# Optimization experiments

Hardware: AMD Instinct MI355X
Metric: run time of the kernel (lower is better)

Reference implementation:

```python
import jax, jax.numpy as jnp
import numpy as np

B, L, S, M, N = 128, 3, 256, 256, 20000
NS, A, NL = 4, 5, 2
MAP_RANGE = 10.0
DELTA_VAR = 0.1
EPS = 1e-5


def _ln(x):
    mu = jnp.mean(x, -1, keepdims=True)
    var = jnp.var(x, -1, keepdims=True)
    return (x - mu) / jnp.sqrt(var + EPS)


def _cal_map_last(map_pts, anchor_last):
    # map_pts: [2, N], anchor_last: [B, 1, L] -> [B, M, 2]
    pos = anchor_last[:, 0, 0:2]
    d = map_pts[None, :, :] - pos[:, :, None]                    # [B,2,N]
    th = anchor_last[:, 0, -1]
    c, s = jnp.cos(th), jnp.sin(th)
    rot = jnp.stack([jnp.stack([c, s], -1), jnp.stack([-s, c], -1)], 1)  # [B,2,2]
    m = jnp.einsum('bij,bjn->bin', rot, d)                       # ego-frame points
    dis = jnp.sqrt(jnp.sum(m * m, axis=1, keepdims=True))        # [B,1,N]
    m = jnp.where(dis >= MAP_RANGE, 1e10, m)
    m = jnp.sort(m, axis=-1)                                     # per-coordinate sort (as in torch)
    m = jnp.where(m >= 1e9, 0.0, m)
    m = m[:, :, :M]                                              # torch F.pad negative pad == crop to map_num_max
    return jnp.transpose(m, (0, 2, 1))


def _forward(inp_start_point, map_pts, end_point, delta_limit_mean,
             W_enc_anchor, Wq, Wk, Wv, W_in, W_out, W_map1, W_map2,
             W_ih0, W_ih1, W_hh0, W_hh1, W_m1, W_m2, W_v1, W_v2):
    anchor = inp_start_point
    var_last = jnp.ones_like(anchor) * 0.01  # never updated, as in torch source
    pre_mean, pre_var, views = [], [], []
    scale = 1.0 / np.sqrt(S)                 # MHA 1 head -> head_dim = S
    bsz = anchor.shape[0]
    for step in range(NS):
        dm, dv = [anchor], [var_last]
        vt = [jnp.transpose(_cal_map_last(map_pts, anchor), (0, 2, 1))]
        h = jnp.ones((NL, bsz, S), anchor.dtype)
        c = jnp.ones((NL, bsz, S), anchor.dtype)
        for _ in range(A - 1):
            enc_a = _ln(jnp.concatenate([anchor, anchor - end_point, var_last], -1) @ W_enc_anchor[step].T)  # [B,1,S]
            ml = jax.lax.stop_gradient(_cal_map_last(map_pts, anchor))  # torch.no_grad in encode_last_map
            q = ml @ Wq[step].T
            k = ml @ Wk[step].T
            v = ml @ Wv[step].T
            wq, wk, wv = jnp.split(W_in[step], 3, axis=0)
            q2 = q @ wq.T
            k2 = k @ wk.T
            v2 = v @ wv.T
            attn = jax.nn.softmax(jnp.einsum('bqs,bks->bqk', q2, k2) * scale, axis=-1)
            o = jnp.einsum('bqk,bks->bqs', attn, v2) @ W_out[step].T    # [B,M,S]
            x = jax.nn.relu(jnp.transpose(o, (0, 2, 1)))                # [B,S,M]
            x = jax.nn.relu(x @ W_map1[step].T) @ W_map2[step].T        # [B,S,1]
            enc_m = _ln(jnp.transpose(x, (0, 2, 1)))                    # [B,1,S]
            xl = jnp.concatenate([enc_a, enc_m], -1)[:, 0, :]           # [B,2S], single LSTM timestep
            hs, cs = [], []
            for l, (Wih, Whh) in enumerate(((W_ih0[step], W_hh0[step]), (W_ih1[step], W_hh1[step]))):
                g = xl @ Wih.T + h[l] @ Whh.T
                i_g, f_g, g_g, o_g = jnp.split(g, 4, -1)               # torch gate order i,f,g,o
                cl = jax.nn.sigmoid(f_g) * c[l] + jax.nn.sigmoid(i_g) * jnp.tanh(g_g)
                hl = jax.nn.sigmoid(o_g) * jnp.tanh(cl)
                hs.append(hl)
                cs.append(cl)
                xl = hl
            h, c = jnp.stack(hs), jnp.stack(cs)
            mn = _ln(xl)[:, None, :]                                    # [B,1,S]
            mean = jnp.tanh(jax.nn.relu(jax.nn.relu(mn) @ W_m1[step].T) @ W_m2[step].T) * delta_limit_mean + anchor
            varr = jax.nn.sigmoid(jax.nn.relu(jax.nn.relu(mn) @ W_v1[step].T) @ W_v2[step].T) * DELTA_VAR
            dm.append(mean)
            dv.append(varr)
            anchor = mean
            vt.append(jnp.transpose(_cal_map_last(map_pts, anchor), (0, 2, 1)))
        pre_mean.append(jnp.concatenate(dm, 1)[:, None])    # [B,1,A,L]
        pre_var.append(jnp.concatenate(dv, 1)[:, None])
        views.append(jnp.stack(vt, 1)[:, None])             # [B,1,A,2,M]
    return (jnp.concatenate(pre_mean, 1), jnp.concatenate(pre_var, 1), jnp.concatenate(views, 1))


def setup_inputs() -> dict:
    key = jax.random.key(0)
    ks = jax.random.split(key, 20)

    def w(k, shape, fan):
        return jax.random.normal(k, shape, jnp.float32) / np.sqrt(fan)

    return {
        'inp_start_point': jax.random.normal(ks[0], (B, 1, L), jnp.float32) * 2.0,
        'map_pts': jax.random.uniform(ks[1], (2, N), jnp.float32, -50.0, 50.0),
        'end_point': jnp.array([5.0, 5.0, 0.0], jnp.float32),
        'delta_limit_mean': jnp.array([1.0, 1.0, 0.3], jnp.float32),
        'W_enc_anchor': w(ks[2], (NS, S, 3 * L), 3 * L),
        'Wq': w(ks[3], (NS, S, 2), 2),
        'Wk': w(ks[4], (NS, S, 2), 2),
        'Wv': w(ks[5], (NS, S, 2), 2),
        'W_in': w(ks[6], (NS, 3 * S, S), S),
        'W_out': w(ks[7], (NS, S, S), S),
        'W_map1': w(ks[8], (NS, S, M), M),
        'W_map2': w(ks[9], (NS, 1, S), S),
        'W_ih0': w(ks[10], (NS, 4 * S, 2 * S), 2 * S),
        'W_ih1': w(ks[11], (NS, 4 * S, S), S),
        'W_hh0': w(ks[12], (NS, 4 * S, S), S),
        'W_hh1': w(ks[13], (NS, 4 * S, S), S),
        'W_m1': w(ks[14], (NS, S, S), S),
        'W_m2': w(ks[15], (NS, L, S), S),
        'W_v1': w(ks[16], (NS, S, S), S),
        'W_v2': w(ks[17], (NS, L, S), S),
    }


def reference(inp_start_point, map_pts, end_point, delta_limit_mean,
              W_enc_anchor, Wq, Wk, Wv, W_in, W_out, W_map1, W_map2,
              W_ih0, W_ih1, W_hh0, W_hh1, W_m1, W_m2, W_v1, W_v2):
    return _forward(inp_start_point, map_pts, end_point, delta_limit_mean,
                    W_enc_anchor, Wq, Wk, Wv, W_in, W_out, W_map1, W_map2,
                    W_ih0, W_ih1, W_hh0, W_hh1, W_m1, W_m2, W_v1, W_v2)
```

## Files before the change

kernel.cpp:

```cpp
#include <hip/hip_runtime.h>

#define BB 128
#define NPTS 20000
#define NSTEP 4
#define NITER 4

#define OFF_ANCHOR 0
#define OFF_G      384
#define OFF_AO     400
#define OFF_U      2448
#define OFF_XL     67984
#define OFF_OUT    133520
#define OFF_H      166288
#define OFF_C      231824
#define OFF_GB     297360
#define OFF_RMN    428432
#define OFF_TM     461200
#define OFF_TV     493968

#define OUT_VAR   7680
#define OUT_VIEWS 15360

__device__ __forceinline__ float sigf(float x){ return 1.0f/(1.0f+expf(-x)); }

__device__ __forceinline__ float blockSum256(float v, float* buf){
    for (int off = 32; off > 0; off >>= 1) v += __shfl_down(v, off, 64);
    int tid = threadIdx.x;
    __syncthreads();
    if ((tid & 63) == 0) buf[tid >> 6] = v;
    __syncthreads();
    return (buf[0] + buf[1]) + (buf[2] + buf[3]);
}

__device__ __forceinline__ double blockSum256d(double v, double* buf){
    for (int off = 32; off > 0; off >>= 1) v += __shfl_down(v, off, 64);
    int tid = threadIdx.x;
    __syncthreads();
    if ((tid & 63) == 0) buf[tid >> 6] = v;
    __syncthreads();
    return (buf[0] + buf[1]) + (buf[2] + buf[3]);
}

__global__ __launch_bounds__(256) void k_init(const float* __restrict__ inp, float* __restrict__ ws)
{
    int i = blockIdx.x*256 + threadIdx.x;
    if (i < BB*3) ws[OFF_ANCHOR + i] = inp[i];
}

__global__ __launch_bounds__(256) void k_pre(const float* __restrict__ Wq, const float* __restrict__ Wk,
                                             const float* __restrict__ Wv, const float* __restrict__ Win,
                                             const float* __restrict__ Wout, float* __restrict__ ws)
{
    __shared__ float wql[512], wkl[512], wvl[512];
    __shared__ double avl[512];
    __shared__ double dbuf[4];
    int s = blockIdx.x, t = threadIdx.x;
    wql[t] = Wq[s*512 + t];   wql[256+t] = Wq[s*512 + 256 + t];
    wkl[t] = Wk[s*512 + t];   wkl[256+t] = Wk[s*512 + 256 + t];
    wvl[t] = Wv[s*512 + t];   wvl[256+t] = Wv[s*512 + 256 + t];
    __syncthreads();
    const float* wq = Win + s*196608 + t*256;
    const float* wk = wq + 65536;
    const float* wv = wq + 131072;
    double aq0=0,aq1=0,ak0=0,ak1=0,av0=0,av1=0;
    for (int j = 0; j < 256; j++){
        double a = wq[j], b = wk[j], c = wv[j];
        aq0 += a*(double)wql[j*2]; aq1 += a*(double)wql[j*2+1];
        ak0 += b*(double)wkl[j*2]; ak1 += b*(double)wkl[j*2+1];
        av0 += c*(double)wvl[j*2]; av1 += c*(double)wvl[j*2+1];
    }
    avl[t*2] = av0; avl[t*2+1] = av1;
    double g00 = blockSum256d(aq0*ak0, dbuf);
    double g01 = blockSum256d(aq0*ak1, dbuf);
    double g10 = blockSum256d(aq1*ak0, dbuf);
    double g11 = blockSum256d(aq1*ak1, dbuf);
    if (t == 0){
        ws[OFF_G + s*4+0] = (float)g00; ws[OFF_G + s*4+1] = (float)g01;
        ws[OFF_G + s*4+2] = (float)g10; ws[OFF_G + s*4+3] = (float)g11;
    }
    const float* wo = Wout + s*65536 + t*256;
    double o0 = 0.0, o1 = 0.0;
    for (int j = 0; j < 256; j++){
        double w = wo[j];
        o0 += w*avl[j*2]; o1 += w*avl[j*2+1];
    }
    ws[OFF_AO + s*512 + t*2]   = (float)o0;
    ws[OFF_AO + s*512 + t*2+1] = (float)o1;
}

__global__ __launch_bounds__(256) void k_step_init(float* __restrict__ ws, float* __restrict__ out, int s)
{
    int gid = blockIdx.x*256 + threadIdx.x;
    if (gid < 2*BB*256){ ws[OFF_H + gid] = 1.0f; ws[OFF_C + gid] = 1.0f; }
    if (gid < BB*3){
        int b = gid/3, j = gid - b*3;
        out[((b*NSTEP + s)*5 + 0)*3 + j] = ws[OFF_ANCHOR + gid];
        out[OUT_VAR + ((b*NSTEP + s)*5 + 0)*3 + j] = 0.01f;
    }
}

__global__ __launch_bounds__(256) void k_map(const float* __restrict__ mp, float* __restrict__ ws,
                                             float* __restrict__ out, int s, int t)
{
    __shared__ unsigned int histx[2048], histy[2048];
    __shared__ float vx[1024], vy[1024];
    __shared__ float candx[512], candy[512];
    __shared__ float sortx[256], sorty[256];
    __shared__ int scanb[256];
    __shared__ int shjx, shjy;
    __shared__ unsigned int cnt_in, cntx, cnty;
    int tid = threadIdx.x, b = blockIdx.x;
    float ax = ws[OFF_ANCHOR + b*3 + 0];
    float ay = ws[OFF_ANCHOR + b*3 + 1];
    float th = ws[OFF_ANCHOR + b*3 + 2];
    float cth = cosf(th), sth = sinf(th);
    for (int i = tid; i < 2048; i += 256){ histx[i] = 0u; histy[i] = 0u; }
    if (tid == 0){ cnt_in = 0u; cntx = 0u; cnty = 0u; }
    __syncthreads();
    for (int i = tid; i < NPTS; i += 256){
        float dx = mp[i] - ax, dy = mp[NPTS + i] - ay;
        float rx = cth*dx + sth*dy;
        float ry = cth*dy - sth*dx;
        float d  = sqrtf(rx*rx + ry*ry);
        if (d < 10.0f){
            unsigned p = atomicAdd(&cnt_in, 1u);
            if (p < 1024u){ vx[p] = rx; vy[p] = ry; }
            int bx = (int)((rx + 10.0f) * 102.4f); bx = min(max(bx, 0), 2047);
            int by = (int)((ry + 10.0f) * 102.4f); by = min(max(by, 0), 2047);
            atomicAdd(&histx[bx], 1u); atomicAdd(&histy[by], 1u);
        }
    }
    __syncthreads();
    int total = (int)min(cnt_in, 1024u);
    int K = min(256, total);
    {
        int part = 0;
        for (int k = 0; k < 8; k++) part += (int)histx[tid*8 + k];
        scanb[tid] = part; __syncthreads();
        for (int off = 1; off < 256; off <<= 1){
            int v = (tid >= off) ? scanb[tid - off] : 0; __syncthreads();
            scanb[tid] += v; __syncthreads();
        }
        int incl = scanb[tid], excl = incl - part;
        if (K > 0 && excl < K && incl >= K){
            int c = excl;
            for (int k = 0; k < 8; k++){ c += (int)histx[tid*8+k]; if (c >= K){ shjx = tid*8+k; break; } }
        }
        if (K == 0 && tid == 0) shjx = -1;
        __syncthreads();
    }
    {
        int part = 0;
        for (int k = 0; k < 8; k++) part += (int)histy[tid*8 + k];
        scanb[tid] = part; __syncthreads();
        for (int off = 1; off < 256; off <<= 1){
            int v = (tid >= off) ? scanb[tid - off] : 0; __syncthreads();
            scanb[tid] += v; __syncthreads();
        }
        int incl = scanb[tid], excl = incl - part;
        if (K > 0 && excl < K && incl >= K){
            int c = excl;
            for (int k = 0; k < 8; k++){ c += (int)histy[tid*8+k]; if (c >= K){ shjy = tid*8+k; break; } }
        }
        if (K == 0 && tid == 0) shjy = -1;
        __syncthreads();
    }
    int jx = shjx, jy = shjy;
    for (int i = tid; i < total; i += 256){
        float v = vx[i];
        int bx = (int)((v + 10.0f)*102.4f); bx = min(max(bx,0),2047);
        if (bx <= jx){ unsigned p = atomicAdd(&cntx,1u); if (p < 512u) candx[p] = v; }
        v = vy[i];
        int by = (int)((v + 10.0f)*102.4f); by = min(max(by,0),2047);
        if (by <= jy){ unsigned p = atomicAdd(&cnty,1u); if (p < 512u) candy[p] = v; }
    }
    __syncthreads();
    int cx = (int)min(cntx, 512u), cy = (int)min(cnty, 512u);
    for (int i = tid; i < cx; i += 256){
        float v = candx[i];
        int r = 0;
        for (int j = 0; j < cx; j++){
            float w = candx[j];
            r += (w < v) || (w == v && j < i);
        }
        if (r < 256) sortx[r] = v;
    }
    for (int i = tid; i < cy; i += 256){
        float v = candy[i];
        int r = 0;
        for (int j = 0; j < cy; j++){
            float w = candy[j];
            r += (w < v) || (w == v && j < i);
        }
        if (r < 256) sorty[r] = v;
    }
    __syncthreads();
    int obase = OUT_VIEWS + (((b*NSTEP + s)*5 + t)*2)*256;
    out[obase + tid]       = (tid < K) ? sortx[tid] : 0.0f;
    out[obase + 256 + tid] = (tid < K) ? sorty[tid] : 0.0f;
}

__global__ __launch_bounds__(256) void k_encattn(const float* __restrict__ out, float* __restrict__ ws,
                                                 const float* __restrict__ Wenc, const float* __restrict__ endp,
                                                 int s, int t)
{
    __shared__ float rbuf[4];
    __shared__ float mlx[256], mly[256];
    int b = blockIdx.x, i = threadIdx.x;
    int obase = OUT_VIEWS + (((b*NSTEP + s)*5 + t)*2)*256;
    mlx[i] = out[obase + i];
    mly[i] = out[obase + 256 + i];
    float a0 = ws[OFF_ANCHOR + b*3+0], a1 = ws[OFF_ANCHOR + b*3+1], a2 = ws[OFF_ANCHOR + b*3+2];
    float z[9] = {a0, a1, a2, a0-endp[0], a1-endp[1], a2-endp[2], 0.01f, 0.01f, 0.01f};
    const float* w = Wenc + s*2304 + i*9;
    float acc = 0.f;
    #pragma unroll
    for (int j = 0; j < 9; j++) acc += z[j]*w[j];
    float mu = blockSum256(acc, rbuf) * (1.0f/256.0f);
    float d = acc - mu;
    float var = blockSum256(d*d, rbuf) * (1.0f/256.0f);
    ws[OFF_XL + b*512 + i] = d * rsqrtf(var + 1e-5f);
    float g00 = ws[OFF_G + s*4+0], g01 = ws[OFF_G + s*4+1];
    float g10 = ws[OFF_G + s*4+2], g11 = ws[OFF_G + s*4+3];
    float x = mlx[i], y = mly[i];
    float t0 = g00*x + g10*y;
    float t1 = g01*x + g11*y;
    float mx = -1e30f;
    for (int j = 0; j < 256; j++){
        float l = (t0*mlx[j] + t1*mly[j]) * 0.0625f;
        mx = fmaxf(mx, l);
    }
    float sum = 0.f, ux = 0.f, uy = 0.f;
    for (int j = 0; j < 256; j++){
        float l = (t0*mlx[j] + t1*mly[j]) * 0.0625f;
        float e = expf(l - mx);
        sum += e; ux += e*mlx[j]; uy += e*mly[j];
    }
    float inv = 1.0f/sum;
    ws[OFF_U + b*512 + i*2]   = ux*inv;
    ws[OFF_U + b*512 + i*2+1] = uy*inv;
}

__global__ __launch_bounds__(256) void k_big(float* __restrict__ ws, const float* __restrict__ W1,
                                             const float* __restrict__ W2, int s)
{
    __shared__ __align__(16) float ul[512];
    __shared__ float aol[128];
    __shared__ float w2l[64];
    __shared__ __align__(16) float xt[64*36];
    __shared__ __align__(16) float w1t[64*36];
    __shared__ float red[64*17];
    int sct = blockIdx.x, st = blockIdx.y, b = blockIdx.z;
    int tid = threadIdx.x, tx = tid & 15, ty = tid >> 4;
    {
        float2 uv = *(const float2*)(ws + OFF_U + b*512 + tid*2);
        ul[tid*2] = uv.x; ul[tid*2+1] = uv.y;
        if (tid < 128) aol[tid] = ws[OFF_AO + s*512 + st*128 + tid];
        if (tid < 64)  w2l[tid] = W2[sct*64 + tid];
    }
    __syncthreads();
    float acc[4][4];
    #pragma unroll
    for (int i=0;i<4;i++){
        #pragma unroll
        for (int j=0;j<4;j++) acc[i][j] = 0.f;
    }
    for (int mt = 0; mt < 8; mt++){
        {
            int cl = tid >> 2, f0 = tid & 3;
            const float* g = W1 + (sct*64 + cl)*256 + mt*32 + f0*4;
            float4 v0 = *(const float4*)g;
            float4 v1 = *(const float4*)(g + 16);
            *(float4*)(w1t + cl*36 + f0*4)      = v0;
            *(float4*)(w1t + cl*36 + f0*4 + 16) = v1;
        }
        {
            int r = tid >> 2, mg = tid & 3;
            float A0 = aol[r*2], A1 = aol[r*2+1];
            int m0 = mt*32 + mg*4;
            float4 o0, o1;
            o0.x = fmaxf(A0*ul[(m0+0)*2] + A1*ul[(m0+0)*2+1], 0.f);
            o0.y = fmaxf(A0*ul[(m0+1)*2] + A1*ul[(m0+1)*2+1], 0.f);
            o0.z = fmaxf(A0*ul[(m0+2)*2] + A1*ul[(m0+2)*2+1], 0.f);
            o0.w = fmaxf(A0*ul[(m0+3)*2] + A1*ul[(m0+3)*2+1], 0.f);
            int m1 = mt*32 + (mg+4)*4;
            o1.x = fmaxf(A0*ul[(m1+0)*2] + A1*ul[(m1+0)*2+1], 0.f);
            o1.y = fmaxf(A0*ul[(m1+1)*2] + A1*ul[(m1+1)*2+1], 0.f);
            o1.z = fmaxf(A0*ul[(m1+2)*2] + A1*ul[(m1+2)*2+1], 0.f);
            o1.w = fmaxf(A0*ul[(m1+3)*2] + A1*ul[(m1+3)*2+1], 0.f);
            *(float4*)(xt + r*36 + mg*4)     = o0;
            *(float4*)(xt + r*36 + (mg+4)*4) = o1;
        }
        __syncthreads();
        #pragma unroll
        for (int m4 = 0; m4 < 8; m4++){
            float4 xv[4], wv[4];
            #pragma unroll
            for (int i=0;i<4;i++) xv[i] = *(const float4*)(xt + (ty*4+i)*36 + m4*4);
            #pragma unroll
            for (int j=0;j<4;j++) wv[j] = *(const float4*)(w1t + (tx + 16*j)*36 + m4*4);
            #pragma unroll
            for (int i=0;i<4;i++){
                #pragma unroll
                for (int j=0;j<4;j++){
                    acc[i][j] += xv[i].x*wv[j].x + xv[i].y*wv[j].y + xv[i].z*wv[j].z + xv[i].w*wv[j].w;
                }
            }
        }
        __syncthreads();
    }
    float psum[4];
    #pragma unroll
    for (int i=0;i<4;i++){
        float p = 0.f;
        #pragma unroll
        for (int j=0;j<4;j++) p += fmaxf(acc[i][j], 0.f) * w2l[tx + 16*j];
        psum[i] = p;
        red[(ty*4+i)*17 + tx] = p;
    }
    __syncthreads();
    if (tid < 64){
        float sm = 0.f;
        #pragma unroll
        for (int q=0;q<16;q++) sm += red[tid*17 + q];
        ws[OFF_GB + b*1024 + sct*256 + st*64 + tid] = sm;
    }
}

__global__ __launch_bounds__(256) void k_lnencm(float* __restrict__ ws)
{
    __shared__ float rbuf[4];
    int b = blockIdx.x, t = threadIdx.x;
    const float* p = ws + OFF_GB + b*1024;
    float v = ((p[t] + p[256+t]) + p[512+t]) + p[768+t];
    v = p[t];
    v += p[256+t]; v += p[512+t]; v += p[768+t];
    float mu = blockSum256(v, rbuf) * (1.0f/256.0f);
    float d = v - mu;
    float var = blockSum256(d*d, rbuf) * (1.0f/256.0f);
    ws[OFF_XL + b*512 + 256 + t] = d * rsqrtf(var + 1e-5f);
}

template<int K>
__device__ __forceinline__ void gemm_pass(const float* __restrict__ A, const float* __restrict__ W,
                                          float* As, float* Wsh, float (&acc)[2][4],
                                          int bt, int ot, int tid)
{
    int tx = tid & 15, ty = tid >> 4;
    for (int kt = 0; kt < K/32; kt++){
        {
            int bb = tid >> 3, kk = (tid & 7) * 4;
            float4 v = *(const float4*)(A + (bt*32+bb)*K + kt*32 + kk);
            float* ap = As + bb*33 + kk;
            ap[0]=v.x; ap[1]=v.y; ap[2]=v.z; ap[3]=v.w;
        }
        {
            int oo = tid >> 2, kk = (tid & 3) * 8;
            const float* g = W + (ot*64+oo)*K + kt*32 + kk;
            float4 v0 = *(const float4*)g;
            float4 v1 = *(const float4*)(g + 4);
            float* wp = Wsh + oo*33 + kk;
            wp[0]=v0.x; wp[1]=v0.y; wp[2]=v0.z; wp[3]=v0.w;
            wp[4]=v1.x; wp[5]=v1.y; wp[6]=v1.z; wp[7]=v1.w;
        }
        __syncthreads();
        #pragma unroll
        for (int kk = 0; kk < 32; kk++){
            float a0 = As[(ty*2)*33 + kk], a1 = As[(ty*2+1)*33 + kk];
            float w0 = Wsh[(tx*4)*33+kk],   w1 = Wsh[(tx*4+1)*33+kk];
            float w2 = Wsh[(tx*4+2)*33+kk], w3 = Wsh[(tx*4+3)*33+kk];
            acc[0][0] += a0*w0; acc[0][1] += a0*w1; acc[0][2] += a0*w2; acc[0][3] += a0*w3;
            acc[1][0] += a1*w0; acc[1][1] += a1*w1; acc[1][2] += a1*w2; acc[1][3] += a1*w3;
        }
        __syncthreads();
    }
}

template<int K1, int K2, int RELU>
__global__ __launch_bounds__(256) void k_gemm(const float* __restrict__ A1, const float* __restrict__ W1,
                                              const float* __restrict__ A2, const float* __restrict__ W2,
                                              float* __restrict__ C, int Osz)
{
    __shared__ float As[32*33];
    __shared__ float Wsh[64*33];
    int tid = threadIdx.x, tx = tid & 15, ty = tid >> 4;
    int ot = blockIdx.x, bt = blockIdx.y;
    float acc[2][4];
    #pragma unroll
    for (int i=0;i<2;i++){
        #pragma unroll
        for (int j=0;j<4;j++) acc[i][j]=0.f;
    }
    gemm_pass<K1>(A1, W1, As, Wsh, acc, bt, ot, tid);
    if constexpr (K2 > 0){
        gemm_pass<K2>(A2, W2, As, Wsh, acc, bt, ot, tid);
    }
    #pragma unroll
    for (int i=0;i<2;i++){
        float4 v;
        v.x = acc[i][0]; v.y = acc[i][1]; v.z = acc[i][2]; v.w = acc[i][3];
        if (RELU){ v.x=fmaxf(v.x,0.f); v.y=fmaxf(v.y,0.f); v.z=fmaxf(v.z,0.f); v.w=fmaxf(v.w,0.f); }
        *(float4*)(C + (bt*32+ty*2+i)*Osz + ot*64 + tx*4) = v;
    }
}

__global__ __launch_bounds__(256) void k_heads2(const float* __restrict__ A, const float* __restrict__ Wm1,
                                                const float* __restrict__ Wv1, float* __restrict__ ws)
{
    __shared__ float As[32*33];
    __shared__ float Wsh[64*33];
    int tid = threadIdx.x, tx = tid & 15, ty = tid >> 4;
    int bx = blockIdx.x, bt = blockIdx.y;
    int ot = bx & 3;
    const float* W = (bx < 4) ? Wm1 : Wv1;
    float* C = ws + ((bx < 4) ? OFF_TM : OFF_TV);
    float acc[2][4];
    #pragma unroll
    for (int i=0;i<2;i++){
        #pragma unroll
        for (int j=0;j<4;j++) acc[i][j]=0.f;
    }
    gemm_pass<256>(A, W, As, Wsh, acc, bt, ot, tid);
    #pragma unroll
    for (int i=0;i<2;i++){
        float4 v;
        v.x = fmaxf(acc[i][0],0.f); v.y = fmaxf(acc[i][1],0.f);
        v.z = fmaxf(acc[i][2],0.f); v.w = fmaxf(acc[i][3],0.f);
        *(float4*)(C + (bt*32+ty*2+i)*256 + ot*64 + tx*4) = v;
    }
}

__global__ __launch_bounds__(256) void k_gates(float* __restrict__ ws, int l)
{
    int b = blockIdx.x, t = threadIdx.x;
    const float* g = ws + OFF_GB + b*1024;
    float ig = g[t], fg = g[256+t], gg = g[512+t], og = g[768+t];
    int idx = l*BB*256 + b*256 + t;
    float cold = ws[OFF_C + idx];
    float cl = sigf(fg)*cold + sigf(ig)*tanhf(gg);
    float hl = sigf(og)*tanhf(cl);
    ws[OFF_C + idx] = cl;
    ws[OFF_H + idx] = hl;
}

__global__ __launch_bounds__(256) void k_mn(float* __restrict__ ws)
{
    __shared__ float rbuf[4];
    int b = blockIdx.x, t = threadIdx.x;
    const float* g = ws + OFF_GB + b*1024;
    float ig = g[t], fg = g[256+t], gg = g[512+t], og = g[768+t];
    int idx = BB*256 + b*256 + t;
    float cold = ws[OFF_C + idx];
    float cl = sigf(fg)*cold + sigf(ig)*tanhf(gg);
    float hl = sigf(og)*tanhf(cl);
    ws[OFF_C + idx] = cl;
    ws[OFF_H + idx] = hl;
    float mu = blockSum256(hl, rbuf) * (1.0f/256.0f);
    float d = hl - mu;
    float var = blockSum256(d*d, rbuf) * (1.0f/256.0f);
    ws[OFF_RMN + b*256 + t] = fmaxf(d * rsqrtf(var + 1e-5f), 0.0f);
}

__global__ __launch_bounds__(256) void k_head(const float* __restrict__ Wm2, const float* __restrict__ Wv2,
                                              const float* __restrict__ dlm, float* __restrict__ ws,
                                              float* __restrict__ out, int s, int t)
{
    int b = blockIdx.x, tid = threadIdx.x;
    int w = tid >> 6, lane = tid & 63;
    #pragma unroll
    for (int p = 0; p < 2; p++){
        int oi = p*4 + w;
        if (oi < 6){
            int j = (oi < 3) ? oi : oi - 3;
            const float* tb = ws + ((oi < 3) ? OFF_TM : OFF_TV) + b*256;
            const float* wr = ((oi < 3) ? Wm2 : Wv2) + j*256;
            float pa = 0.f;
            #pragma unroll
            for (int q = 0; q < 4; q++) pa += tb[lane + 64*q] * wr[lane + 64*q];
            for (int off = 32; off > 0; off >>= 1) pa += __shfl_down(pa, off, 64);
            if (lane == 0){
                if (oi < 3){
                    float mv = tanhf(pa) * dlm[j] + ws[OFF_ANCHOR + b*3 + j];
                    out[((b*NSTEP + s)*5 + (t+1))*3 + j] = mv;
                    ws[OFF_ANCHOR + b*3 + j] = mv;
                } else {
                    out[OUT_VAR + ((b*NSTEP + s)*5 + (t+1))*3 + j] = sigf(pa)*0.1f;
                }
            }
        }
    }
}

extern "C" void kernel_launch(void* const* d_in, const int* in_sizes, int n_in,
                              void* d_out, int out_size, void* d_ws, size_t ws_size,
                              hipStream_t stream)
{
    (void)in_sizes; (void)n_in; (void)out_size; (void)ws_size;
    const float* inp  = (const float*)d_in[0];
    const float* mp   = (const float*)d_in[1];
    const float* endp = (const float*)d_in[2];
    const float* dlm  = (const float*)d_in[3];
    const float* Wenc = (const float*)d_in[4];
    const float* Wq   = (const float*)d_in[5];
    const float* Wk   = (const float*)d_in[6];
    const float* Wv   = (const float*)d_in[7];
    const float* Win  = (const float*)d_in[8];
    const float* Wout = (const float*)d_in[9];
    const float* Wmap1= (const float*)d_in[10];
    const float* Wmap2= (const float*)d_in[11];
    const float* Wih0 = (const float*)d_in[12];
    const float* Wih1 = (const float*)d_in[13];
    const float* Whh0 = (const float*)d_in[14];
    const float* Whh1 = (const float*)d_in[15];
    const float* Wm1  = (const float*)d_in[16];
    const float* Wm2  = (const float*)d_in[17];
    const float* Wv1  = (const float*)d_in[18];
    const float* Wv2  = (const float*)d_in[19];
    float* out = (float*)d_out;
    float* ws  = (float*)d_ws;

    k_init<<<2, 256, 0, stream>>>(inp, ws);
    k_pre<<<NSTEP, 256, 0, stream>>>(Wq, Wk, Wv, Win, Wout, ws);
    for (int s = 0; s < NSTEP; s++){
        k_step_init<<<256, 256, 0, stream>>>(ws, out, s);
        for (int t = 0; t < NITER; t++){
            k_map<<<BB, 256, 0, stream>>>(mp, ws, out, s, t);
            k_encattn<<<BB, 256, 0, stream>>>(out, ws, Wenc, endp, s, t);
            k_big<<<dim3(4, 4, BB), 256, 0, stream>>>(ws, Wmap1 + s*65536, Wmap2 + s*256, s);
            k_lnencm<<<BB, 256, 0, stream>>>(ws);
            k_gemm<512,256,0><<<dim3(16,4), 256, 0, stream>>>(ws+OFF_XL, Wih0 + s*524288,
                                                              ws+OFF_H,  Whh0 + s*262144,
                                                              ws+OFF_GB, 1024);
            k_gates<<<BB, 256, 0, stream>>>(ws, 0);
            k_gemm<256,256,0><<<dim3(16,4), 256, 0, stream>>>(ws+OFF_H,          Wih1 + s*262144,
                                                              ws+OFF_H + BB*256, Whh1 + s*262144,
                                                              ws+OFF_GB, 1024);
            k_mn<<<BB, 256, 0, stream>>>(ws);
            k_heads2<<<dim3(8,4), 256, 0, stream>>>(ws+OFF_RMN, Wm1 + s*65536, Wv1 + s*65536, ws);
            k_head<<<BB, 256, 0, stream>>>(Wm2 + s*768, Wv2 + s*768, dlm, ws, out, s, t);
        }
        k_map<<<BB, 256, 0, stream>>>(mp, ws, out, s, 4);
    }
}
```

Baseline: 4.492 ms.

## Fuse map sort with encoder/attention, coarsen histogram, enlarge k_big tiles

The map selection kernel, the encoder/attention kernel and the per-step init are merged into one kernel, so the views no longer round-trip through global memory. The final map of each step is now computed by the next step's first launch, which writes it to both slots. The radix histogram drops from 2048 to 256 bins with a single scan, and the candidate buffer shrinks to 448. k_big moves to 128x128 tiles with an 8x8 register tile per thread, which cuts the grid from 16 to 4 blocks per batch row but raises register pressure, and a coarser histogram risks candidate overflow.

```diff
diff --git a/kernel.cpp b/kernel.cpp
--- a/kernel.cpp
+++ b/kernel.cpp
@@ -10,7 +10,6 @@
 #define OFF_AO     400
 #define OFF_U      2448
 #define OFF_XL     67984
-#define OFF_OUT    133520
 #define OFF_H      166288
 #define OFF_C      231824
 #define OFF_GB     297360
@@ -88,33 +87,24 @@
     ws[OFF_AO + s*512 + t*2+1] = (float)o1;
 }
 
-__global__ __launch_bounds__(256) void k_step_init(float* __restrict__ ws, float* __restrict__ out, int s)
-{
-    int gid = blockIdx.x*256 + threadIdx.x;
-    if (gid < 2*BB*256){ ws[OFF_H + gid] = 1.0f; ws[OFF_C + gid] = 1.0f; }
-    if (gid < BB*3){
-        int b = gid/3, j = gid - b*3;
-        out[((b*NSTEP + s)*5 + 0)*3 + j] = ws[OFF_ANCHOR + gid];
-        out[OUT_VAR + ((b*NSTEP + s)*5 + 0)*3 + j] = 0.01f;
-    }
-}
-
-__global__ __launch_bounds__(256) void k_map(const float* __restrict__ mp, float* __restrict__ ws,
-                                             float* __restrict__ out, int s, int t)
-{
-    __shared__ unsigned int histx[2048], histy[2048];
+__global__ __launch_bounds__(256) void k_mapenc(const float* __restrict__ mp, float* __restrict__ ws,
+                                                float* __restrict__ out, const float* __restrict__ Wenc,
+                                                const float* __restrict__ endp, int s, int t, int wprev)
+{
+    __shared__ unsigned int histx[256], histy[256];
     __shared__ float vx[1024], vy[1024];
-    __shared__ float candx[512], candy[512];
-    __shared__ float sortx[256], sorty[256];
-    __shared__ int scanb[256];
+    __shared__ float candx[448], candy[448];
+    __shared__ float mxS[256], myS[256];
+    __shared__ int scanx[256], scany[256];
     __shared__ int shjx, shjy;
     __shared__ unsigned int cnt_in, cntx, cnty;
+    __shared__ float rbuf[4];
     int tid = threadIdx.x, b = blockIdx.x;
     float ax = ws[OFF_ANCHOR + b*3 + 0];
     float ay = ws[OFF_ANCHOR + b*3 + 1];
     float th = ws[OFF_ANCHOR + b*3 + 2];
     float cth = cosf(th), sth = sinf(th);
-    for (int i = tid; i < 2048; i += 256){ histx[i] = 0u; histy[i] = 0u; }
+    histx[tid] = 0u; histy[tid] = 0u;
     if (tid == 0){ cnt_in = 0u; cntx = 0u; cnty = 0u; }
     __syncthreads();
     for (int i = tid; i < NPTS; i += 256){
@@ -125,205 +115,201 @@
         if (d < 10.0f){
             unsigned p = atomicAdd(&cnt_in, 1u);
             if (p < 1024u){ vx[p] = rx; vy[p] = ry; }
-            int bx = (int)((rx + 10.0f) * 102.4f); bx = min(max(bx, 0), 2047);
-            int by = (int)((ry + 10.0f) * 102.4f); by = min(max(by, 0), 2047);
+            int bx = min(max((int)((rx + 10.0f)*12.8f), 0), 255);
+            int by = min(max((int)((ry + 10.0f)*12.8f), 0), 255);
             atomicAdd(&histx[bx], 1u); atomicAdd(&histy[by], 1u);
         }
     }
     __syncthreads();
     int total = (int)min(cnt_in, 1024u);
     int K = min(256, total);
-    {
-        int part = 0;
-        for (int k = 0; k < 8; k++) part += (int)histx[tid*8 + k];
-        scanb[tid] = part; __syncthreads();
-        for (int off = 1; off < 256; off <<= 1){
-            int v = (tid >= off) ? scanb[tid - off] : 0; __syncthreads();
-            scanb[tid] += v; __syncthreads();
-        }
-        int incl = scanb[tid], excl = incl - part;
-        if (K > 0 && excl < K && incl >= K){
-            int c = excl;
-            for (int k = 0; k < 8; k++){ c += (int)histx[tid*8+k]; if (c >= K){ shjx = tid*8+k; break; } }
-        }
-        if (K == 0 && tid == 0) shjx = -1;
+    int px = (int)histx[tid], py = (int)histy[tid];
+    scanx[tid] = px; scany[tid] = py;
+    __syncthreads();
+    for (int off = 1; off < 256; off <<= 1){
+        int vxs = (tid >= off) ? scanx[tid - off] : 0;
+        int vys = (tid >= off) ? scany[tid - off] : 0;
         __syncthreads();
-    }
-    {
-        int part = 0;
-        for (int k = 0; k < 8; k++) part += (int)histy[tid*8 + k];
-        scanb[tid] = part; __syncthreads();
-        for (int off = 1; off < 256; off <<= 1){
-            int v = (tid >= off) ? scanb[tid - off] : 0; __syncthreads();
-            scanb[tid] += v; __syncthreads();
-        }
-        int incl = scanb[tid], excl = incl - part;
-        if (K > 0 && excl < K && incl >= K){
-            int c = excl;
-            for (int k = 0; k < 8; k++){ c += (int)histy[tid*8+k]; if (c >= K){ shjy = tid*8+k; break; } }
-        }
-        if (K == 0 && tid == 0) shjy = -1;
+        scanx[tid] += vxs; scany[tid] += vys;
         __syncthreads();
     }
+    if (K > 0){
+        if (scanx[tid] - px < K && scanx[tid] >= K) shjx = tid;
+        if (scany[tid] - py < K && scany[tid] >= K) shjy = tid;
+    } else if (tid == 0){ shjx = -1; shjy = -1; }
+    __syncthreads();
     int jx = shjx, jy = shjy;
     for (int i = tid; i < total; i += 256){
         float v = vx[i];
-        int bx = (int)((v + 10.0f)*102.4f); bx = min(max(bx,0),2047);
-        if (bx <= jx){ unsigned p = atomicAdd(&cntx,1u); if (p < 512u) candx[p] = v; }
+        int bx = min(max((int)((v + 10.0f)*12.8f), 0), 255);
+        if (bx <= jx){ unsigned p = atomicAdd(&cntx, 1u); if (p < 448u) candx[p] = v; }
         v = vy[i];
-        int by = (int)((v + 10.0f)*102.4f); by = min(max(by,0),2047);
-        if (by <= jy){ unsigned p = atomicAdd(&cnty,1u); if (p < 512u) candy[p] = v; }
-    }
-    __syncthreads();
-    int cx = (int)min(cntx, 512u), cy = (int)min(cnty, 512u);
+        int by = min(max((int)((v + 10.0f)*12.8f), 0), 255);
+        if (by <= jy){ unsigned p = atomicAdd(&cnty, 1u); if (p < 448u) candy[p] = v; }
+    }
+    __syncthreads();
+    int cx = (int)min(cntx, 448u), cy = (int)min(cnty, 448u);
     for (int i = tid; i < cx; i += 256){
         float v = candx[i];
         int r = 0;
-        for (int j = 0; j < cx; j++){
-            float w = candx[j];
-            r += (w < v) || (w == v && j < i);
-        }
-        if (r < 256) sortx[r] = v;
+        for (int j2 = 0; j2 < cx; j2++){
+            float w2 = candx[j2];
+            r += (w2 < v) || (w2 == v && j2 < i);
+        }
+        if (r < 256) mxS[r] = v;
     }
     for (int i = tid; i < cy; i += 256){
         float v = candy[i];
         int r = 0;
-        for (int j = 0; j < cy; j++){
-            float w = candy[j];
-            r += (w < v) || (w == v && j < i);
-        }
-        if (r < 256) sorty[r] = v;
-    }
-    __syncthreads();
+        for (int j2 = 0; j2 < cy; j2++){
+            float w2 = candy[j2];
+            r += (w2 < v) || (w2 == v && j2 < i);
+        }
+        if (r < 256) myS[r] = v;
+    }
+    __syncthreads();
+    float mlx = (tid < K) ? mxS[tid] : 0.0f;
+    float mly = (tid < K) ? myS[tid] : 0.0f;
     int obase = OUT_VIEWS + (((b*NSTEP + s)*5 + t)*2)*256;
-    out[obase + tid]       = (tid < K) ? sortx[tid] : 0.0f;
-    out[obase + 256 + tid] = (tid < K) ? sorty[tid] : 0.0f;
-}
-
-__global__ __launch_bounds__(256) void k_encattn(const float* __restrict__ out, float* __restrict__ ws,
-                                                 const float* __restrict__ Wenc, const float* __restrict__ endp,
-                                                 int s, int t)
-{
-    __shared__ float rbuf[4];
-    __shared__ float mlx[256], mly[256];
-    int b = blockIdx.x, i = threadIdx.x;
-    int obase = OUT_VIEWS + (((b*NSTEP + s)*5 + t)*2)*256;
-    mlx[i] = out[obase + i];
-    mly[i] = out[obase + 256 + i];
-    float a0 = ws[OFF_ANCHOR + b*3+0], a1 = ws[OFF_ANCHOR + b*3+1], a2 = ws[OFF_ANCHOR + b*3+2];
-    float z[9] = {a0, a1, a2, a0-endp[0], a1-endp[1], a2-endp[2], 0.01f, 0.01f, 0.01f};
-    const float* w = Wenc + s*2304 + i*9;
+    out[obase + tid]       = mlx;
+    out[obase + 256 + tid] = mly;
+    if (wprev){
+        int pbase = OUT_VIEWS + (((b*NSTEP + (s-1))*5 + 4)*2)*256;
+        out[pbase + tid]       = mlx;
+        out[pbase + 256 + tid] = mly;
+    }
+    if (t == 4) return;
+    __syncthreads();
+    mxS[tid] = mlx; myS[tid] = mly;
+    float a0 = ax, a1 = ay, a2 = th;
+    float z9[9] = {a0, a1, a2, a0-endp[0], a1-endp[1], a2-endp[2], 0.01f, 0.01f, 0.01f};
+    const float* w = Wenc + s*2304 + tid*9;
     float acc = 0.f;
     #pragma unroll
-    for (int j = 0; j < 9; j++) acc += z[j]*w[j];
+    for (int j2 = 0; j2 < 9; j2++) acc += z9[j2]*w[j2];
     float mu = blockSum256(acc, rbuf) * (1.0f/256.0f);
-    float d = acc - mu;
-    float var = blockSum256(d*d, rbuf) * (1.0f/256.0f);
-    ws[OFF_XL + b*512 + i] = d * rsqrtf(var + 1e-5f);
+    float dd = acc - mu;
+    float var = blockSum256(dd*dd, rbuf) * (1.0f/256.0f);
+    ws[OFF_XL + b*512 + tid] = dd * rsqrtf(var + 1e-5f);
     float g00 = ws[OFF_G + s*4+0], g01 = ws[OFF_G + s*4+1];
     float g10 = ws[OFF_G + s*4+2], g11 = ws[OFF_G + s*4+3];
-    float x = mlx[i], y = mly[i];
-    float t0 = g00*x + g10*y;
-    float t1 = g01*x + g11*y;
-    float mx = -1e30f;
-    for (int j = 0; j < 256; j++){
-        float l = (t0*mlx[j] + t1*mly[j]) * 0.0625f;
-        mx = fmaxf(mx, l);
+    float xq = mxS[tid], yq = myS[tid];
+    float t0 = g00*xq + g10*yq;
+    float t1 = g01*xq + g11*yq;
+    float mxv = -1e30f;
+    for (int j2 = 0; j2 < 256; j2++){
+        float l = (t0*mxS[j2] + t1*myS[j2]) * 0.0625f;
+        mxv = fmaxf(mxv, l);
     }
     float sum = 0.f, ux = 0.f, uy = 0.f;
-    for (int j = 0; j < 256; j++){
-        float l = (t0*mlx[j] + t1*mly[j]) * 0.0625f;
-        float e = expf(l - mx);
-        sum += e; ux += e*mlx[j]; uy += e*mly[j];
+    for (int j2 = 0; j2 < 256; j2++){
+        float l = (t0*mxS[j2] + t1*myS[j2]) * 0.0625f;
+        float e = expf(l - mxv);
+        sum += e; ux += e*mxS[j2]; uy += e*myS[j2];
     }
     float inv = 1.0f/sum;
-    ws[OFF_U + b*512 + i*2]   = ux*inv;
-    ws[OFF_U + b*512 + i*2+1] = uy*inv;
+    ws[OFF_U + b*512 + tid*2]   = ux*inv;
+    ws[OFF_U + b*512 + tid*2+1] = uy*inv;
+    if (t == 0){
+        ws[OFF_H + b*256 + tid] = 1.0f;
+        ws[OFF_H + BB*256 + b*256 + tid] = 1.0f;
+        ws[OFF_C + b*256 + tid] = 1.0f;
+        ws[OFF_C + BB*256 + b*256 + tid] = 1.0f;
+        if (tid < 3){
+            out[((b*NSTEP + s)*5 + 0)*3 + tid] = ws[OFF_ANCHOR + b*3 + tid];
+            out[OUT_VAR + ((b*NSTEP + s)*5 + 0)*3 + tid] = 0.01f;
+        }
+    }
 }
 
 __global__ __launch_bounds__(256) void k_big(float* __restrict__ ws, const float* __restrict__ W1,
                                              const float* __restrict__ W2, int s)
 {
     __shared__ __align__(16) float ul[512];
-    __shared__ float aol[128];
-    __shared__ float w2l[64];
-    __shared__ __align__(16) float xt[64*36];
-    __shared__ __align__(16) float w1t[64*36];
-    __shared__ float red[64*17];
-    int sct = blockIdx.x, st = blockIdx.y, b = blockIdx.z;
+    __shared__ float aol[256];
+    __shared__ float w2l[128];
+    __shared__ __align__(16) float xt[128*36];
+    __shared__ __align__(16) float w1t[128*36];
+    int jc = blockIdx.x, sc = blockIdx.y, b = blockIdx.z;
     int tid = threadIdx.x, tx = tid & 15, ty = tid >> 4;
     {
         float2 uv = *(const float2*)(ws + OFF_U + b*512 + tid*2);
         ul[tid*2] = uv.x; ul[tid*2+1] = uv.y;
-        if (tid < 128) aol[tid] = ws[OFF_AO + s*512 + st*128 + tid];
-        if (tid < 64)  w2l[tid] = W2[sct*64 + tid];
-    }
-    __syncthreads();
-    float acc[4][4];
-    #pragma unroll
-    for (int i=0;i<4;i++){
-        #pragma unroll
-        for (int j=0;j<4;j++) acc[i][j] = 0.f;
-    }
+        aol[tid] = ws[OFF_AO + s*512 + sc*256 + tid];
+        if (tid < 128) w2l[tid] = W2[jc*128 + tid];
+    }
+    __syncthreads();
+    float acc[8][8];
+    #pragma unroll
+    for (int i=0;i<8;i++){
+        #pragma unroll
+        for (int j=0;j<8;j++) acc[i][j] = 0.f;
+    }
+    int row2 = tid >> 1, mh = (tid & 1)*16;
     for (int mt = 0; mt < 8; mt++){
         {
-            int cl = tid >> 2, f0 = tid & 3;
-            const float* g = W1 + (sct*64 + cl)*256 + mt*32 + f0*4;
+            const float* g = W1 + (jc*128 + row2)*256 + mt*32 + mh;
             float4 v0 = *(const float4*)g;
-            float4 v1 = *(const float4*)(g + 16);
-            *(float4*)(w1t + cl*36 + f0*4)      = v0;
-            *(float4*)(w1t + cl*36 + f0*4 + 16) = v1;
+            float4 v1 = *(const float4*)(g + 4);
+            float4 v2 = *(const float4*)(g + 8);
+            float4 v3 = *(const float4*)(g + 12);
+            float* wp = w1t + row2*36 + mh;
+            *(float4*)(wp)      = v0;
+            *(float4*)(wp + 4)  = v1;
+            *(float4*)(wp + 8)  = v2;
+            *(float4*)(wp + 12) = v3;
         }
         {
-            int r = tid >> 2, mg = tid & 3;
-            float A0 = aol[r*2], A1 = aol[r*2+1];
-            int m0 = mt*32 + mg*4;
-            float4 o0, o1;
-            o0.x = fmaxf(A0*ul[(m0+0)*2] + A1*ul[(m0+0)*2+1], 0.f);
-            o0.y = fmaxf(A0*ul[(m0+1)*2] + A1*ul[(m0+1)*2+1], 0.f);
-            o0.z = fmaxf(A0*ul[(m0+2)*2] + A1*ul[(m0+2)*2+1], 0.f);
-            o0.w = fmaxf(A0*ul[(m0+3)*2] + A1*ul[(m0+3)*2+1], 0.f);
-            int m1 = mt*32 + (mg+4)*4;
-            o1.x = fmaxf(A0*ul[(m1+0)*2] + A1*ul[(m1+0)*2+1], 0.f);
-            o1.y = fmaxf(A0*ul[(m1+1)*2] + A1*ul[(m1+1)*2+1], 0.f);
-            o1.z = fmaxf(A0*ul[(m1+2)*2] + A1*ul[(m1+2)*2+1], 0.f);
-            o1.w = fmaxf(A0*ul[(m1+3)*2] + A1*ul[(m1+3)*2+1], 0.f);
-            *(float4*)(xt + r*36 + mg*4)     = o0;
-            *(float4*)(xt + r*36 + (mg+4)*4) = o1;
+            float A0 = aol[row2*2], A1 = aol[row2*2+1];
+            float* xp = xt + row2*36 + mh;
+            #pragma unroll
+            for (int q = 0; q < 4; q++){
+                int m0 = mt*32 + mh + q*4;
+                float4 o0;
+                o0.x = fmaxf(A0*ul[(m0+0)*2] + A1*ul[(m0+0)*2+1], 0.f);
+                o0.y = fmaxf(A0*ul[(m0+1)*2] + A1*ul[(m0+1)*2+1], 0.f);
+                o0.z = fmaxf(A0*ul[(m0+2)*2] + A1*ul[(m0+2)*2+1], 0.f);
+                o0.w = fmaxf(A0*ul[(m0+3)*2] + A1*ul[(m0+3)*2+1], 0.f);
+                *(float4*)(xp + q*4) = o0;
+            }
         }
         __syncthreads();
         #pragma unroll
         for (int m4 = 0; m4 < 8; m4++){
-            float4 xv[4], wv[4];
+            float4 xv[8], wv[8];
             #pragma unroll
-            for (int i=0;i<4;i++) xv[i] = *(const float4*)(xt + (ty*4+i)*36 + m4*4);
+            for (int i=0;i<8;i++) xv[i] = *(const float4*)(xt + (ty + 16*i)*36 + m4*4);
             #pragma unroll
-            for (int j=0;j<4;j++) wv[j] = *(const float4*)(w1t + (tx + 16*j)*36 + m4*4);
+            for (int j=0;j<8;j++) wv[j] = *(const float4*)(w1t + (tx + 16*j)*36 + m4*4);
             #pragma unroll
-            for (int i=0;i<4;i++){
+            for (int i=0;i<8;i++){
                 #pragma unroll
-                for (int j=0;j<4;j++){
+                for (int j=0;j<8;j++){
                     acc[i][j] += xv[i].x*wv[j].x + xv[i].y*wv[j].y + xv[i].z*wv[j].z + xv[i].w*wv[j].w;
                 }
             }
         }
         __syncthreads();
     }
-    float psum[4];
-    #pragma unroll
-    for (int i=0;i<4;i++){
-        float p = 0.f;
-        #pragma unroll
-        for (int j=0;j<4;j++) p += fmaxf(acc[i][j], 0.f) * w2l[tx + 16*j];
-        psum[i] = p;
-        red[(ty*4+i)*17 + tx] = p;
-    }
-    __syncthreads();
-    if (tid < 64){
+    float* red = w1t;
+    #pragma unroll
+    for (int i=0;i<8;i++){
+        #pragma unroll
+        for (int ch=0;ch<2;ch++){
+            float p = 0.f;
+            #pragma unroll
+            for (int jj=0;jj<4;jj++)
+                p += fmaxf(acc[i][ch*4+jj], 0.f) * w2l[ch*64 + tx + 16*jj];
+            red[((ty + 16*i)*2 + ch)*16 + tx] = p;
+        }
+    }
+    __syncthreads();
+    {
+        int row = tid & 127, ch = tid >> 7;
         float sm = 0.f;
         #pragma unroll
-        for (int q=0;q<16;q++) sm += red[tid*17 + q];
-        ws[OFF_GB + b*1024 + sct*256 + st*64 + tid] = sm;
+        for (int q=0;q<16;q++) sm += red[(row*2 + ch)*16 + q];
+        ws[OFF_GB + b*1024 + (jc*2 + ch)*256 + sc*128 + row] = sm;
     }
 }
 
@@ -332,8 +318,7 @@
     __shared__ float rbuf[4];
     int b = blockIdx.x, t = threadIdx.x;
     const float* p = ws + OFF_GB + b*1024;
-    float v = ((p[t] + p[256+t]) + p[512+t]) + p[768+t];
-    v = p[t];
+    float v = p[t];
     v += p[256+t]; v += p[512+t]; v += p[768+t];
     float mu = blockSum256(v, rbuf) * (1.0f/256.0f);
     float d = v - mu;
@@ -522,11 +507,10 @@
     k_init<<<2, 256, 0, stream>>>(inp, ws);
     k_pre<<<NSTEP, 256, 0, stream>>>(Wq, Wk, Wv, Win, Wout, ws);
     for (int s = 0; s < NSTEP; s++){
-        k_step_init<<<256, 256, 0, stream>>>(ws, out, s);
         for (int t = 0; t < NITER; t++){
-            k_map<<<BB, 256, 0, stream>>>(mp, ws, out, s, t);
-            k_encattn<<<BB, 256, 0, stream>>>(out, ws, Wenc, endp, s, t);
-            k_big<<<dim3(4, 4, BB), 256, 0, stream>>>(ws, Wmap1 + s*65536, Wmap2 + s*256, s);
+            k_mapenc<<<BB, 256, 0, stream>>>(mp, ws, out, Wenc, endp, s, t,
+                                             (t == 0 && s > 0) ? 1 : 0);
+            k_big<<<dim3(2, 2, BB), 256, 0, stream>>>(ws, Wmap1 + s*65536, Wmap2 + s*256, s);
             k_lnencm<<<BB, 256, 0, stream>>>(ws);
             k_gemm<512,256,0><<<dim3(16,4), 256, 0, stream>>>(ws+OFF_XL, Wih0 + s*524288,
                                                               ws+OFF_H,  Whh0 + s*262144,
@@ -539,6 +523,6 @@
             k_heads2<<<dim3(8,4), 256, 0, stream>>>(ws+OFF_RMN, Wm1 + s*65536, Wv1 + s*65536, ws);
             k_head<<<BB, 256, 0, stream>>>(Wm2 + s*768, Wv2 + s*768, dlm, ws, out, s, t);
         }
-        k_map<<<BB, 256, 0, stream>>>(mp, ws, out, s, 4);
-    }
-}
+    }
+    k_mapenc<<<BB, 256, 0, stream>>>(mp, ws, out, Wenc, endp, 3, 4, 0);
+}
```

Result: slower. 8.502 ms (+89.3%).
